# Performance work log

Measured on AMD Instinct MI355X. Metric: run time of the kernel, lower is better.

The kernel has to match this reference:

```python
import jax, jax.numpy as jnp
import numpy as np
import math

S, B, H, NH, I, L, V, BK, MP = 512, 8, 768, 12, 2304, 4, 16384, 32, 512
DH = H // NH   # 64
DV = I // NH   # 192
EPS = 1e-7
SCALE = 1.0 / math.sqrt(3 * DH)


def make_log_bucket_position(relative_pos, bucket_size, max_position):
    sign = np.sign(relative_pos)
    mid = bucket_size // 2
    abs_pos = np.where((relative_pos < mid) & (relative_pos > -mid),
                       mid - 1,
                       np.clip(np.abs(relative_pos), None, max_position - 1))
    log_pos = np.ceil(np.log(abs_pos / mid) / math.log((max_position - 1) / mid) * (mid - 1)).astype(np.int64) + mid
    bucket_pos = np.where(abs_pos <= mid, relative_pos, log_pos * sign).astype(np.int64)
    return bucket_pos


def layer_norm(x, eps=EPS):
    m = jnp.mean(x, axis=-1, keepdims=True)
    v = jnp.var(x, axis=-1, keepdims=True)
    return (x - m) / jnp.sqrt(v + eps)


def setup_inputs() -> dict:
    key = jax.random.key(0)
    ks = jax.random.split(key, 10)
    std = math.sqrt(2.0 / (5.0 * H))
    inp = {}
    inp['input_ids'] = jax.random.randint(ks[0], (S, B), 0, V, dtype=jnp.int32)
    inp['attention_mask'] = jnp.zeros((B, 1, 1, S), dtype=bool)
    rel = np.arange(S)[:, None] - np.arange(S)[None, :]
    rel = make_log_bucket_position(rel, BK, MP)
    inp['position_indices'] = jnp.asarray(BK - 1 + rel, dtype=jnp.int32)  # [S,S] in [0, 2*BK-2]
    inp['word_emb'] = jax.random.normal(ks[1], (V, H), jnp.float32) * std
    inp['rel_emb'] = jax.random.normal(ks[2], (2 * BK - 1, H), jnp.float32) * std
    inp['rel_ln_w'] = jnp.ones((H,), jnp.float32)
    inp['rel_ln_b'] = jnp.zeros((H,), jnp.float32)
    inp['Wv'] = jax.random.normal(ks[3], (L, 2 * I, H), jnp.float32) * std
    inp['Wqk'] = jax.random.normal(ks[4], (L, 2 * H, H), jnp.float32) * std
    inp['bqk'] = jnp.zeros((L, 2 * H), jnp.float32)
    inp['Wo'] = jax.random.normal(ks[5], (L, H, I), jnp.float32) * std
    inp['l_skip'] = jnp.zeros((L, I), jnp.float32)
    return inp


def attention_glu_layer(x, mask, rel, pos_idx, Wv, Wqk, bqk, Wo, l_skip):
    # x: [S,B,H]; rel: [2*BK-1, H]; mask: [B,1,1,S] bool (True = masked)
    h = layer_norm(x)
    vg = jnp.einsum('sbh,ih->sbi', h, Wv)                  # [S,B,2I]
    value, gate = jnp.split(vg, 2, axis=-1)
    gate = jax.nn.gelu(gate, approximate=False)
    value_skip = jax.nn.gelu(value, approximate=False)
    qk = jnp.einsum('sbh,ih->sbi', h, Wqk) + bqk            # [S,B,2H]
    q, k = jnp.split(qk, 2, axis=-1)
    # relative position projections
    pos = rel @ Wqk.T + bqk                                 # [2*BK-1, 2H]
    pos = pos[pos_idx]                                      # [S,S,2H]
    q_pos, k_pos = jnp.split(pos, 2, axis=-1)
    q_pos = q_pos.reshape(S, S, NH, DH)
    k_pos = k_pos.reshape(S, S, NH, DH)
    q4 = q.reshape(S, B, NH, DH)
    k4 = k.reshape(S, B, NH, DH)
    v4 = value.reshape(S, B, NH, DV)
    scores = jnp.einsum('qbhd,kbhd->bhqk', q4, k4) * SCALE
    scores = scores + jnp.einsum('qbhd,qkhd->bhqk', q4, k_pos) * SCALE
    scores = scores + jnp.einsum('kbhd,qkhd->bhqk', k4, q_pos) * SCALE
    scores = jnp.where(mask, -jnp.inf, scores)
    probs = jax.nn.softmax(scores, axis=-1)
    probs = jnp.where(mask, 0.0, probs)
    ctx = jnp.einsum('bhqk,kbhv->qbhv', probs, v4).reshape(S, B, I)
    ctx = ctx + jax.nn.sigmoid(l_skip) * value_skip
    ctx = ctx * gate
    ctx = layer_norm(ctx)
    out = jnp.einsum('sbi,hi->sbh', ctx, Wo)
    return x + out


def reference(input_ids, attention_mask, position_indices, word_emb, rel_emb,
              rel_ln_w, rel_ln_b, Wv, Wqk, bqk, Wo, l_skip):
    x = layer_norm(word_emb[input_ids])                      # [S,B,H]
    rel = layer_norm(rel_emb) * rel_ln_w + rel_ln_b          # [2*BK-1, H]
    for l in range(L):
        x = attention_glu_layer(x, attention_mask, rel, position_indices,
                                Wv[l], Wqk[l], bqk[l], Wo[l], l_skip[l])
    return x
```

## Files before the change

### kernel.cpp

```cpp
#include <hip/hip_runtime.h>
#include <hip/hip_bf16.h>
#include <math.h>

#define S 512
#define B 8
#define H 768
#define NH 12
#define DH 64
#define DV 192
#define II 2304
#define NL 4
#define SCALE 0.07216878364870322f
#define EPS 1e-7f

typedef __attribute__((ext_vector_type(8))) short short8;
typedef __attribute__((ext_vector_type(4))) float f32x4;

__device__ __forceinline__ float b2f(ushort u){
  union { float f; unsigned int u; } v; v.u = ((unsigned int)u) << 16; return v.f;
}
__device__ __forceinline__ ushort f2b(float f){
  union { float f; unsigned int u; } v; v.f = f;
  unsigned int u = v.u;
  return (ushort)((u + 0x7fffu + ((u >> 16) & 1u)) >> 16);
}
__device__ __forceinline__ float gelu_f(float x){
  return 0.5f * x * (1.0f + erff(x * 0.70710678118654752f));
}
__device__ __forceinline__ void async_copy16(const ushort* g, ushort* l){
  __builtin_amdgcn_global_load_lds(
      (const __attribute__((address_space(1))) void*)g,
      (__attribute__((address_space(3))) void*)l, 16, 0, 0);
}

__device__ __forceinline__ void block_sum2(float& s, float& s2, float* red, int t){
  #pragma unroll
  for(int off=32; off>=1; off>>=1){ s += __shfl_xor(s, off); s2 += __shfl_xor(s2, off); }
  int w = t >> 6;
  if((t & 63) == 0){ red[w] = s; red[4 + w] = s2; }
  __syncthreads();
  s  = red[0] + red[1] + red[2] + red[3];
  s2 = red[4] + red[5] + red[6] + red[7];
}

__global__ __launch_bounds__(256)
void f2b_kernel(const float* __restrict__ in, ushort* __restrict__ out){
  int i = (blockIdx.x * 256 + threadIdx.x) * 4;
  float4 v = *(const float4*)(in + i);
  __attribute__((aligned(8))) ushort tmp[4] = { f2b(v.x), f2b(v.y), f2b(v.z), f2b(v.w) };
  *(uint2*)(out + i) = *(const uint2*)tmp;
}

__global__ __launch_bounds__(256)
void embed_ln_kernel(const int* __restrict__ ids, const float* __restrict__ wemb,
                     float* __restrict__ x)
{
  __shared__ float red[8];
  const int sb = blockIdx.x, t = threadIdx.x;
  const float* row = wemb + (size_t)ids[sb] * H;
  float v0 = row[t], v1 = row[t+256], v2 = row[t+512];
  float s = v0+v1+v2, s2 = v0*v0+v1*v1+v2*v2;
  block_sum2(s, s2, red, t);
  float mean = s * (1.0f/H);
  float rstd = rsqrtf(s2*(1.0f/H) - mean*mean + EPS);
  float* xo = x + (size_t)sb * H;
  xo[t]     = (v0-mean)*rstd;
  xo[t+256] = (v1-mean)*rstd;
  xo[t+512] = (v2-mean)*rstd;
}

__global__ __launch_bounds__(256)
void rel_ln_kernel(const float* __restrict__ rel_emb, const float* __restrict__ w,
                   const float* __restrict__ bia, ushort* __restrict__ outb)
{
  __shared__ float red[8];
  const int j = blockIdx.x, t = threadIdx.x;
  const float* row = rel_emb + (size_t)j * H;
  float v0=row[t], v1=row[t+256], v2=row[t+512];
  float s=v0+v1+v2, s2=v0*v0+v1*v1+v2*v2;
  block_sum2(s,s2,red,t);
  float mean = s*(1.0f/H);
  float rstd = rsqrtf(s2*(1.0f/H)-mean*mean+EPS);
  ushort* o = outb + (size_t)j*H;
  o[t]     = f2b((v0-mean)*rstd * w[t]     + bia[t]);
  o[t+256] = f2b((v1-mean)*rstd * w[t+256] + bia[t+256]);
  o[t+512] = f2b((v2-mean)*rstd * w[t+512] + bia[t+512]);
}

__global__ __launch_bounds__(256)
void ln_x_kernel(const float* __restrict__ x, ushort* __restrict__ h)
{
  __shared__ float red[8];
  const int sb = blockIdx.x, t = threadIdx.x;
  const float* row = x + (size_t)sb * H;
  float v0 = row[t], v1 = row[t+256], v2 = row[t+512];
  float s = v0+v1+v2, s2 = v0*v0+v1*v1+v2*v2;
  block_sum2(s, s2, red, t);
  float mean = s * (1.0f/H);
  float rstd = rsqrtf(s2*(1.0f/H) - mean*mean + EPS);
  ushort* o = h + (size_t)sb * H;
  o[t]     = f2b((v0-mean)*rstd);
  o[t+256] = f2b((v1-mean)*rstd);
  o[t+512] = f2b((v2-mean)*rstd);
}

__global__ __launch_bounds__(256)
void gemm_nt64(const ushort* __restrict__ A, const ushort* __restrict__ Bw,
               const float* __restrict__ bias, ushort* __restrict__ Cout,
               int M, int N, int K)
{
  __shared__ ushort As[64][40];
  __shared__ ushort Bs[64][40];
  const int n0 = blockIdx.x * 64, m0 = blockIdx.y * 64;
  const int t = threadIdx.x;
  const int lrow = t >> 2, lk = (t & 3) * 8;
  const int lane = t & 63, w = t >> 6, lr = lane & 15, lq = lane >> 4;
  const int wr = (w >> 1) * 32, wc = (w & 1) * 32;
  f32x4 z = {0.f,0.f,0.f,0.f};
  f32x4 acc[2][2] = {{z,z},{z,z}};
  const int arow = m0 + lrow;
  const ushort* aptr = A  + (size_t)arow * K + lk;
  const ushort* bptr = Bw + (size_t)(n0 + lrow) * K + lk;
  for(int k0 = 0; k0 < K; k0 += 32){
    short8 av = {0,0,0,0,0,0,0,0};
    if(arow < M) av = *(const short8*)(aptr + k0);
    short8 bv = *(const short8*)(bptr + k0);
    __syncthreads();
    *(short8*)&As[lrow][lk] = av;
    *(short8*)&Bs[lrow][lk] = bv;
    __syncthreads();
    short8 a0 = *(const short8*)&As[wr + lr][lq * 8];
    short8 a1 = *(const short8*)&As[wr + 16 + lr][lq * 8];
    short8 b0 = *(const short8*)&Bs[wc + lr][lq * 8];
    short8 b1 = *(const short8*)&Bs[wc + 16 + lr][lq * 8];
    acc[0][0] = __builtin_amdgcn_mfma_f32_16x16x32_bf16(a0, b0, acc[0][0], 0,0,0);
    acc[0][1] = __builtin_amdgcn_mfma_f32_16x16x32_bf16(a0, b1, acc[0][1], 0,0,0);
    acc[1][0] = __builtin_amdgcn_mfma_f32_16x16x32_bf16(a1, b0, acc[1][0], 0,0,0);
    acc[1][1] = __builtin_amdgcn_mfma_f32_16x16x32_bf16(a1, b1, acc[1][1], 0,0,0);
  }
  #pragma unroll
  for(int i=0;i<2;i++){
    #pragma unroll
    for(int j=0;j<2;j++){
      #pragma unroll
      for(int r=0;r<4;r++){
        int m = m0 + wr + i*16 + lq*4 + r;
        int n = n0 + wc + j*16 + lr;
        if(m >= M) continue;
        float v = acc[i][j][r];
        if(bias) v += bias[n];
        Cout[(size_t)m*N + n] = f2b(v);
      }
    }
  }
}

template<int OUT_MODE>
__global__ __launch_bounds__(256)
void gemm128(const ushort* __restrict__ A, const ushort* __restrict__ Bw,
             const float* __restrict__ bias, void* __restrict__ Cout,
             int M, int N, int K)
{
  __shared__ ushort As[128*32];
  __shared__ ushort Bs[128*32];
  const int t = threadIdx.x, w = t>>6, lane = t&63, lr = lane&15, lq = lane>>4;
  const int m0 = blockIdx.y*128, n0 = blockIdx.x*128;
  const int wr = (w>>1)*64, wc = (w&1)*64;
  const int srow = (w*2)*16 + (lane>>2);
  const int sk = (lane&3)*8;
  const ushort* aG = A  + (size_t)(m0+srow)*K + sk;
  const ushort* bG = Bw + (size_t)(n0+srow)*K + sk;
  ushort* aL0 = As + (w*2)*512;
  ushort* aL1 = As + (w*2+1)*512;
  ushort* bL0 = Bs + (w*2)*512;
  ushort* bL1 = Bs + (w*2+1)*512;
  f32x4 z = {0.f,0.f,0.f,0.f};
  f32x4 acc[4][4] = {{z,z,z,z},{z,z,z,z},{z,z,z,z},{z,z,z,z}};
  for(int k0 = 0; k0 < K; k0 += 32){
    __syncthreads();
    async_copy16(aG + k0,                 aL0);
    async_copy16(aG + k0 + (size_t)16*K,  aL1);
    async_copy16(bG + k0,                 bL0);
    async_copy16(bG + k0 + (size_t)16*K,  bL1);
    __syncthreads();
    short8 af[4], bf[4];
    #pragma unroll
    for(int i=0;i<4;i++) af[i] = *(const short8*)&As[(wr + i*16 + lr)*32 + lq*8];
    #pragma unroll
    for(int j=0;j<4;j++) bf[j] = *(const short8*)&Bs[(wc + j*16 + lr)*32 + lq*8];
    #pragma unroll
    for(int i=0;i<4;i++)
      #pragma unroll
      for(int j=0;j<4;j++)
        acc[i][j] = __builtin_amdgcn_mfma_f32_16x16x32_bf16(af[i], bf[j], acc[i][j], 0,0,0);
  }
  #pragma unroll
  for(int i=0;i<4;i++){
    #pragma unroll
    for(int j=0;j<4;j++){
      #pragma unroll
      for(int r=0;r<4;r++){
        int m = m0 + wr + i*16 + lq*4 + r;
        int n = n0 + wc + j*16 + lr;
        float v = acc[i][j][r];
        if(bias) v += bias[n];
        if(OUT_MODE == 0)      ((float*) Cout)[(size_t)m*N + n] = v;
        else if(OUT_MODE == 1) ((ushort*)Cout)[(size_t)m*N + n] = f2b(v);
        else                   ((float*) Cout)[(size_t)m*N + n] += v;
      }
    }
  }
}

__global__ __launch_bounds__(256)
void gemm_vgqk(const ushort* __restrict__ A, const ushort* __restrict__ Ww,
               const float* __restrict__ bqk, ushort* __restrict__ vg,
               ushort* __restrict__ qk)
{
  const int K = H;
  __shared__ ushort As[128*32];
  __shared__ ushort Bs[128*32];
  const int t = threadIdx.x, w = t>>6, lane = t&63, lr = lane&15, lq = lane>>4;
  const int m0 = blockIdx.y*128, n0 = blockIdx.x*128;
  const int wr = (w>>1)*64, wc = (w&1)*64;
  const int srow = (w*2)*16 + (lane>>2);
  const int sk = (lane&3)*8;
  const ushort* aG = A  + (size_t)(m0+srow)*K + sk;
  const ushort* bG = Ww + (size_t)(n0+srow)*K + sk;
  ushort* aL0 = As + (w*2)*512;
  ushort* aL1 = As + (w*2+1)*512;
  ushort* bL0 = Bs + (w*2)*512;
  ushort* bL1 = Bs + (w*2+1)*512;
  f32x4 z = {0.f,0.f,0.f,0.f};
  f32x4 acc[4][4] = {{z,z,z,z},{z,z,z,z},{z,z,z,z},{z,z,z,z}};
  for(int k0 = 0; k0 < K; k0 += 32){
    __syncthreads();
    async_copy16(aG + k0,                 aL0);
    async_copy16(aG + k0 + (size_t)16*K,  aL1);
    async_copy16(bG + k0,                 bL0);
    async_copy16(bG + k0 + (size_t)16*K,  bL1);
    __syncthreads();
    short8 af[4], bf[4];
    #pragma unroll
    for(int i=0;i<4;i++) af[i] = *(const short8*)&As[(wr + i*16 + lr)*32 + lq*8];
    #pragma unroll
    for(int j=0;j<4;j++) bf[j] = *(const short8*)&Bs[(wc + j*16 + lr)*32 + lq*8];
    #pragma unroll
    for(int i=0;i<4;i++)
      #pragma unroll
      for(int j=0;j<4;j++)
        acc[i][j] = __builtin_amdgcn_mfma_f32_16x16x32_bf16(af[i], bf[j], acc[i][j], 0,0,0);
  }
  const bool is_qk = (n0 >= 2*II);
  #pragma unroll
  for(int i=0;i<4;i++){
    #pragma unroll
    for(int j=0;j<4;j++){
      #pragma unroll
      for(int r=0;r<4;r++){
        int m = m0 + wr + i*16 + lq*4 + r;
        int n = n0 + wc + j*16 + lr;
        float v = acc[i][j][r];
        if(is_qk){
          int nq = n - 2*II;
          qk[(size_t)m*(2*H) + nq] = f2b(v + bqk[nq]);
        } else {
          vg[(size_t)m*(2*II) + n] = f2b(v);
        }
      }
    }
  }
}

__global__ __launch_bounds__(256)
void cpq_mfma2_kernel(const ushort* __restrict__ qk, const ushort* __restrict__ posb,
                      ushort* __restrict__ cpT, ushort* __restrict__ cqT)
{
  const int kc = blockIdx.x;
  const int bh = blockIdx.y;
  const int bb = bh / NH, h = bh - bb*NH;
  const int which = blockIdx.z;
  const int t = threadIdx.x, w = t>>6, lane = t&63, lr = lane&15, lq = lane>>4;
  const ushort* ab = posb + (size_t)(w*16 + lr)*1536 + (which ? 0 : 768) + h*64;
  short8 a0 = *(const short8*)(ab + lq*8);
  short8 a1 = *(const short8*)(ab + 32 + lq*8);
  f32x4 z = {0.f,0.f,0.f,0.f};
  f32x4 acc[8] = {z,z,z,z,z,z,z,z};
  #pragma unroll
  for(int nt=0; nt<8; nt++){
    const int k = kc*128 + nt*16 + lr;
    const ushort* bp = qk + ((size_t)k*B + bb)*1536 + (which ? 768 : 0) + h*64;
    short8 b0 = *(const short8*)(bp + lq*8);
    short8 b1 = *(const short8*)(bp + 32 + lq*8);
    acc[nt] = __builtin_amdgcn_mfma_f32_16x16x32_bf16(a0, b0, acc[nt], 0,0,0);
    acc[nt] = __builtin_amdgcn_mfma_f32_16x16x32_bf16(a1, b1, acc[nt], 0,0,0);
  }
  ushort* outp = which ? cqT : cpT;
  #pragma unroll
  for(int nt=0; nt<8; nt++){
    #pragma unroll
    for(int r=0;r<4;r++){
      int j = w*16 + lq*4 + r;
      int k = kc*128 + nt*16 + lr;
      outp[((size_t)bh*64 + j)*512 + k] = f2b(acc[nt][r]);
    }
  }
}

__global__ __launch_bounds__(256)
void vt_kernel(const ushort* __restrict__ vg, ushort* __restrict__ vt)
{
  const int st = blockIdx.x, hh = blockIdx.y, b = blockIdx.z;
  __shared__ ushort tile[32][200];
  const int t = threadIdx.x;
  {
    int sl = t >> 3, v0 = (t & 7) * 24;
    const ushort* src = vg + ((size_t)((st*32 + sl)*B + b))*(2*II) + hh*DV + v0;
    *(short8*)&tile[sl][v0]      = *(const short8*)(src);
    *(short8*)&tile[sl][v0 + 8]  = *(const short8*)(src + 8);
    *(short8*)&tile[sl][v0 + 16] = *(const short8*)(src + 16);
  }
  __syncthreads();
  if(t < DV){
    __attribute__((aligned(16))) ushort tmp[32];
    #pragma unroll
    for(int s2=0;s2<32;s2++) tmp[s2] = tile[s2][t];
    ushort* dst = vt + (((size_t)(b*NH + hh))*DV + t)*S + st*32;
    #pragma unroll
    for(int c=0;c<32;c+=8) *(short8*)(dst + c) = *(const short8*)&tmp[c];
  }
}

__global__ __launch_bounds__(256)
void attn_kernel(const ushort* __restrict__ qk, const ushort* __restrict__ vt,
                 const ushort* __restrict__ cpT, const ushort* __restrict__ cqT,
                 const int* __restrict__ pidx, ushort* __restrict__ ctx)
{
  const int bh = blockIdx.x, qt = blockIdx.y;
  const int b = bh / NH, hh = bh - b*NH;
  __shared__ ushort Qs[16][72];
  __shared__ ushort Ps[16][520];
  __shared__ float cps[16][65];
  __shared__ float redm[4][16];
  __shared__ float reds[4][16];
  __shared__ float rowinv[16];
  const int t = threadIdx.x, w = t>>6, lane = t&63, lr = lane&15, lq = lane>>4;

  {
    int r = t >> 4, d0 = (t & 15) * 4;
    const ushort* src = qk + ((size_t)((qt*16 + r)*B + b))*1536 + hh*DH + d0;
    *(uint2*)&Qs[r][d0] = *(const uint2*)src;
  }
  for(int i=t; i<16*64; i+=256){
    int j = i >> 4, r = i & 15;
    cps[r][j] = b2f(cpT[((size_t)bh*64 + j)*512 + qt*16 + r]);
  }
  __syncthreads();

  float sc[8][4];
  const int kbase = w * 128;
  const ushort* cqbase = cqT + (size_t)bh*64*512;
  #pragma unroll
  for(int tile=0; tile<8; tile++){
    const int k0 = kbase + tile*16;
    const ushort* kp = qk + ((size_t)((k0 + lr)*B + b))*1536 + H + hh*DH + lq*8;
    short8 b0 = *(const short8*)kp;
    short8 b1 = *(const short8*)(kp + 32);
    short8 a0 = *(const short8*)&Qs[lr][lq*8];
    short8 a1 = *(const short8*)&Qs[lr][32 + lq*8];
    f32x4 acc = {0.f,0.f,0.f,0.f};
    acc = __builtin_amdgcn_mfma_f32_16x16x32_bf16(a0, b0, acc, 0,0,0);
    acc = __builtin_amdgcn_mfma_f32_16x16x32_bf16(a1, b1, acc, 0,0,0);
    const int kcol = k0 + lr;
    #pragma unroll
    for(int r=0;r<4;r++){
      int ql = lq*4 + r;
      int pi = pidx[(qt*16+ql)*S + kcol];
      sc[tile][r] = (acc[r] + cps[ql][pi]
                     + b2f(cqbase[(size_t)pi*512 + kcol])) * SCALE;
    }
  }

  float gm[4], gs[4];
  #pragma unroll
  for(int r=0;r<4;r++){
    float m = sc[0][r];
    #pragma unroll
    for(int tile=1;tile<8;tile++) m = fmaxf(m, sc[tile][r]);
    #pragma unroll
    for(int off=1; off<16; off<<=1) m = fmaxf(m, __shfl_xor(m, off));
    if(lr==0) redm[w][lq*4+r] = m;
  }
  __syncthreads();
  #pragma unroll
  for(int r=0;r<4;r++){
    int row = lq*4+r;
    gm[r] = fmaxf(fmaxf(redm[0][row],redm[1][row]),fmaxf(redm[2][row],redm[3][row]));
  }
  #pragma unroll
  for(int r=0;r<4;r++){
    float s = 0.f;
    #pragma unroll
    for(int tile=0;tile<8;tile++){ float e = __expf(sc[tile][r]-gm[r]); sc[tile][r]=e; s+=e; }
    #pragma unroll
    for(int off=1; off<16; off<<=1) s += __shfl_xor(s, off);
    if(lr==0) reds[w][lq*4+r] = s;
  }
  __syncthreads();
  #pragma unroll
  for(int r=0;r<4;r++){
    int row = lq*4+r;
    gs[r] = reds[0][row]+reds[1][row]+reds[2][row]+reds[3][row];
    if(w==0 && lr==0) rowinv[row] = 1.0f/gs[r];
  }
  #pragma unroll
  for(int tile=0;tile<8;tile++){
    #pragma unroll
    for(int r=0;r<4;r++) Ps[lq*4+r][kbase + tile*16 + lr] = f2b(sc[tile][r]);
  }
  __syncthreads();

  f32x4 z = {0.f,0.f,0.f,0.f};
  f32x4 acc2[3] = {z,z,z};
  const ushort* vbase = vt + ((size_t)bh)*DV*S;
  for(int kk=0; kk<S; kk+=32){
    short8 a = *(const short8*)&Ps[lr][kk + lq*8];
    #pragma unroll
    for(int ti=0; ti<3; ti++){
      const int v0 = (w*3 + ti)*16;
      short8 bv = *(const short8*)(vbase + (size_t)(v0 + lr)*S + kk + lq*8);
      acc2[ti] = __builtin_amdgcn_mfma_f32_16x16x32_bf16(a, bv, acc2[ti], 0,0,0);
    }
  }
  #pragma unroll
  for(int ti=0; ti<3; ti++){
    const int v0 = (w*3 + ti)*16;
    #pragma unroll
    for(int r=0;r<4;r++){
      int ql = lq*4 + r;
      float val = acc2[ti][r] * rowinv[ql];
      ctx[((size_t)((qt*16+ql)*B + b))*II + hh*DV + v0 + lr] = f2b(val);
    }
  }
}

__global__ __launch_bounds__(256)
void glu_ln_kernel(const ushort* __restrict__ ctx, const ushort* __restrict__ vg,
                   const float* __restrict__ ls, ushort* __restrict__ outb)
{
  __shared__ float red[8];
  const int sb = blockIdx.x, t = threadIdx.x;
  const ushort* crow = ctx + (size_t)sb*II;
  const ushort* vrow = vg + (size_t)sb*2*II;
  float c[9]; float s=0.f, s2=0.f;
  #pragma unroll
  for(int i=0;i<9;i++){
    int idx = t + i*256;
    float cv  = b2f(crow[idx]);
    float val = b2f(vrow[idx]);
    float gt  = b2f(vrow[II + idx]);
    float sk  = 1.0f/(1.0f + __expf(-ls[idx]));
    cv = (cv + sk*gelu_f(val)) * gelu_f(gt);
    c[i]=cv; s+=cv; s2+=cv*cv;
  }
  block_sum2(s,s2,red,t);
  float mean = s*(1.0f/II);
  float rstd = rsqrtf(s2*(1.0f/II)-mean*mean+EPS);
  ushort* o = outb + (size_t)sb*II;
  #pragma unroll
  for(int i=0;i<9;i++) o[t+i*256] = f2b((c[i]-mean)*rstd);
}

__global__ __launch_bounds__(256)
void copy_kernel(const float* __restrict__ x, float* __restrict__ out){
  int i = (blockIdx.x*256 + threadIdx.x)*4;
  *(float4*)(out + i) = *(const float4*)(x + i);
}

extern "C" void kernel_launch(void* const* d_in, const int* in_sizes, int n_in,
                              void* d_out, int out_size, void* d_ws, size_t ws_size,
                              hipStream_t stream)
{
  (void)in_sizes; (void)n_in; (void)out_size; (void)ws_size;
  const int* ids      = (const int*)d_in[0];
  const int* pidx     = (const int*)d_in[2];
  const float* wemb   = (const float*)d_in[3];
  const float* rele   = (const float*)d_in[4];
  const float* rlw    = (const float*)d_in[5];
  const float* rlb    = (const float*)d_in[6];
  const float* Wv     = (const float*)d_in[7];
  const float* Wqk    = (const float*)d_in[8];
  const float* bqk    = (const float*)d_in[9];
  const float* Wo     = (const float*)d_in[10];
  const float* lskip  = (const float*)d_in[11];

  char* wsb = (char*)d_ws;
  float*  x     = (float*) (wsb + 0);
  ushort* h     = (ushort*)(wsb + 12582912);
  ushort* relb  = (ushort*)(wsb + 18874368);
  ushort* posb  = (ushort*)(wsb + 18972672);
  ushort* vg    = (ushort*)(wsb + 19169280);
  ushort* qk    = (ushort*)(wsb + 56918016);
  ushort* cpT   = (ushort*)(wsb + 69500928);
  ushort* cqT   = (ushort*)(wsb + 75792384);
  ushort* ctx   = (ushort*)(wsb + 82083840);
  ushort* vt    = (ushort*)(wsb + 100958208);
  ushort* ctxln = vt;
  ushort* wvqk  = (ushort*)(wsb + 119832576);
  ushort* wqkb  = wvqk + (size_t)(2*II)*H;
  ushort* wob   = (ushort*)(wsb + 129269760);

  embed_ln_kernel<<<S*B, 256, 0, stream>>>(ids, wemb, x);
  rel_ln_kernel<<<63, 256, 0, stream>>>(rele, rlw, rlb, relb);

  for(int l=0; l<NL; l++){
    const float* Wv_l  = Wv  + (size_t)l * (2*II) * H;
    const float* Wqk_l = Wqk + (size_t)l * (2*H) * H;
    const float* bqk_l = bqk + (size_t)l * (2*H);
    const float* Wo_l  = Wo  + (size_t)l * H * II;
    const float* ls_l  = lskip + (size_t)l * II;

    f2b_kernel<<<(2*II*H)/1024, 256, 0, stream>>>(Wv_l, wvqk);
    f2b_kernel<<<(2*H*H)/1024, 256, 0, stream>>>(Wqk_l, wqkb);
    f2b_kernel<<<(H*II)/1024, 256, 0, stream>>>(Wo_l, wob);

    ln_x_kernel<<<S*B, 256, 0, stream>>>(x, h);
    gemm_vgqk<<<dim3((2*II+2*H)/128, (S*B)/128), 256, 0, stream>>>(h, wvqk, bqk_l, vg, qk);
    gemm_nt64<<<dim3((2*H)/64, 1), 256, 0, stream>>>(relb, wqkb, bqk_l, posb, 63, 2*H, H);
    cpq_mfma2_kernel<<<dim3(S/128, B*NH, 2), 256, 0, stream>>>(qk, posb, cpT, cqT);
    vt_kernel<<<dim3(S/32, NH, B), 256, 0, stream>>>(vg, vt);
    attn_kernel<<<dim3(B*NH, S/16), 256, 0, stream>>>(qk, vt, cpT, cqT, pidx, ctx);
    glu_ln_kernel<<<S*B, 256, 0, stream>>>(ctx, vg, ls_l, ctxln);
    gemm128<2><<<dim3(H/128, (S*B)/128), 256, 0, stream>>>(ctxln, wob, nullptr, x, S*B, H, II);
  }
  copy_kernel<<<(S*B*H)/1024, 256, 0, stream>>>(x, (float*)d_out);
}
```

Before: 1.471 ms.

## Process 32 query rows per attention block and merge weight-conversion launches

The attention kernel now handles 32 query rows per block instead of 16, so each K tile and each V tile loaded from global memory feeds two MFMA row-groups. This halves K/V global traffic per query and halves the grid size. The three per-layer fp32-to-bf16 weight conversions are merged into one launch that writes a contiguous buffer. The trade-off is more LDS and registers per block (sc doubles to 64 floats), which may lower occupancy, and fewer blocks to spread across CUs.

```diff
diff --git a/kernel.cpp b/kernel.cpp
--- a/kernel.cpp
+++ b/kernel.cpp
@@ -13,6 +13,10 @@
 #define SCALE 0.07216878364870322f
 #define EPS 1e-7f
 
+#define NW0 (2*II*H)
+#define NW1 (2*H*H)
+#define NW2 (H*II)
+
 typedef __attribute__((ext_vector_type(8))) short short8;
 typedef __attribute__((ext_vector_type(4))) float f32x4;
 
@@ -44,9 +48,14 @@
 }
 
 __global__ __launch_bounds__(256)
-void f2b_kernel(const float* __restrict__ in, ushort* __restrict__ out){
+void f2b3_kernel(const float* __restrict__ in0, const float* __restrict__ in1,
+                 const float* __restrict__ in2, ushort* __restrict__ out){
   int i = (blockIdx.x * 256 + threadIdx.x) * 4;
-  float4 v = *(const float4*)(in + i);
+  const float* src; int off;
+  if(i < NW0){ src = in0; off = i; }
+  else if(i < NW0+NW1){ src = in1; off = i - NW0; }
+  else { src = in2; off = i - NW0 - NW1; }
+  float4 v = *(const float4*)(src + off);
   __attribute__((aligned(8))) ushort tmp[4] = { f2b(v.x), f2b(v.y), f2b(v.z), f2b(v.w) };
   *(uint2*)(out + i) = *(const uint2*)tmp;
 }
@@ -338,108 +347,125 @@
 {
   const int bh = blockIdx.x, qt = blockIdx.y;
   const int b = bh / NH, hh = bh - b*NH;
-  __shared__ ushort Qs[16][72];
-  __shared__ ushort Ps[16][520];
-  __shared__ float cps[16][65];
-  __shared__ float redm[4][16];
-  __shared__ float reds[4][16];
-  __shared__ float rowinv[16];
+  __shared__ ushort Qs[32][72];
+  __shared__ ushort Ps[32][520];
+  __shared__ float cps[32][65];
+  __shared__ float redm[4][32];
+  __shared__ float reds[4][32];
+  __shared__ float rowinv[32];
   const int t = threadIdx.x, w = t>>6, lane = t&63, lr = lane&15, lq = lane>>4;
 
-  {
-    int r = t >> 4, d0 = (t & 15) * 4;
-    const ushort* src = qk + ((size_t)((qt*16 + r)*B + b))*1536 + hh*DH + d0;
+  for(int i=t; i<512; i+=256){
+    int r = i >> 4, d0 = (i & 15) * 4;
+    const ushort* src = qk + ((size_t)((qt*32 + r)*B + b))*1536 + hh*DH + d0;
     *(uint2*)&Qs[r][d0] = *(const uint2*)src;
   }
-  for(int i=t; i<16*64; i+=256){
-    int j = i >> 4, r = i & 15;
-    cps[r][j] = b2f(cpT[((size_t)bh*64 + j)*512 + qt*16 + r]);
+  for(int i=t; i<32*64; i+=256){
+    int j = i >> 5, r = i & 31;
+    cps[r][j] = b2f(cpT[((size_t)bh*64 + j)*512 + qt*32 + r]);
   }
   __syncthreads();
 
-  float sc[8][4];
+  short8 a00 = *(const short8*)&Qs[lr][lq*8];
+  short8 a01 = *(const short8*)&Qs[lr][32 + lq*8];
+  short8 a10 = *(const short8*)&Qs[16 + lr][lq*8];
+  short8 a11 = *(const short8*)&Qs[16 + lr][32 + lq*8];
+
+  float sc[8][8];
   const int kbase = w * 128;
   const ushort* cqbase = cqT + (size_t)bh*64*512;
+  f32x4 z4 = {0.f,0.f,0.f,0.f};
   #pragma unroll
   for(int tile=0; tile<8; tile++){
     const int k0 = kbase + tile*16;
     const ushort* kp = qk + ((size_t)((k0 + lr)*B + b))*1536 + H + hh*DH + lq*8;
     short8 b0 = *(const short8*)kp;
     short8 b1 = *(const short8*)(kp + 32);
-    short8 a0 = *(const short8*)&Qs[lr][lq*8];
-    short8 a1 = *(const short8*)&Qs[lr][32 + lq*8];
-    f32x4 acc = {0.f,0.f,0.f,0.f};
-    acc = __builtin_amdgcn_mfma_f32_16x16x32_bf16(a0, b0, acc, 0,0,0);
-    acc = __builtin_amdgcn_mfma_f32_16x16x32_bf16(a1, b1, acc, 0,0,0);
+    f32x4 acc[2] = {z4, z4};
+    acc[0] = __builtin_amdgcn_mfma_f32_16x16x32_bf16(a00, b0, acc[0], 0,0,0);
+    acc[0] = __builtin_amdgcn_mfma_f32_16x16x32_bf16(a01, b1, acc[0], 0,0,0);
+    acc[1] = __builtin_amdgcn_mfma_f32_16x16x32_bf16(a10, b0, acc[1], 0,0,0);
+    acc[1] = __builtin_amdgcn_mfma_f32_16x16x32_bf16(a11, b1, acc[1], 0,0,0);
     const int kcol = k0 + lr;
     #pragma unroll
-    for(int r=0;r<4;r++){
-      int ql = lq*4 + r;
-      int pi = pidx[(qt*16+ql)*S + kcol];
-      sc[tile][r] = (acc[r] + cps[ql][pi]
-                     + b2f(cqbase[(size_t)pi*512 + kcol])) * SCALE;
-    }
-  }
-
-  float gm[4], gs[4];
-  #pragma unroll
-  for(int r=0;r<4;r++){
-    float m = sc[0][r];
-    #pragma unroll
-    for(int tile=1;tile<8;tile++) m = fmaxf(m, sc[tile][r]);
+    for(int qs=0;qs<2;qs++){
+      #pragma unroll
+      for(int r=0;r<4;r++){
+        int ql = qs*16 + lq*4 + r;
+        int pi = pidx[(qt*32+ql)*S + kcol];
+        sc[tile][qs*4+r] = (acc[qs][r] + cps[ql][pi]
+                       + b2f(cqbase[(size_t)pi*512 + kcol])) * SCALE;
+      }
+    }
+  }
+
+  float gm[8];
+  #pragma unroll
+  for(int j=0;j<8;j++){
+    float m = sc[0][j];
+    #pragma unroll
+    for(int tile=1;tile<8;tile++) m = fmaxf(m, sc[tile][j]);
     #pragma unroll
     for(int off=1; off<16; off<<=1) m = fmaxf(m, __shfl_xor(m, off));
-    if(lr==0) redm[w][lq*4+r] = m;
+    if(lr==0) redm[w][(j>>2)*16 + lq*4 + (j&3)] = m;
   }
   __syncthreads();
   #pragma unroll
-  for(int r=0;r<4;r++){
-    int row = lq*4+r;
-    gm[r] = fmaxf(fmaxf(redm[0][row],redm[1][row]),fmaxf(redm[2][row],redm[3][row]));
-  }
-  #pragma unroll
-  for(int r=0;r<4;r++){
+  for(int j=0;j<8;j++){
+    int ql = (j>>2)*16 + lq*4 + (j&3);
+    gm[j] = fmaxf(fmaxf(redm[0][ql],redm[1][ql]),fmaxf(redm[2][ql],redm[3][ql]));
+  }
+  #pragma unroll
+  for(int j=0;j<8;j++){
     float s = 0.f;
     #pragma unroll
-    for(int tile=0;tile<8;tile++){ float e = __expf(sc[tile][r]-gm[r]); sc[tile][r]=e; s+=e; }
+    for(int tile=0;tile<8;tile++){ float e = __expf(sc[tile][j]-gm[j]); sc[tile][j]=e; s+=e; }
     #pragma unroll
     for(int off=1; off<16; off<<=1) s += __shfl_xor(s, off);
-    if(lr==0) reds[w][lq*4+r] = s;
+    if(lr==0) reds[w][(j>>2)*16 + lq*4 + (j&3)] = s;
   }
   __syncthreads();
   #pragma unroll
-  for(int r=0;r<4;r++){
-    int row = lq*4+r;
-    gs[r] = reds[0][row]+reds[1][row]+reds[2][row]+reds[3][row];
-    if(w==0 && lr==0) rowinv[row] = 1.0f/gs[r];
+  for(int j=0;j<8;j++){
+    int ql = (j>>2)*16 + lq*4 + (j&3);
+    float g = reds[0][ql]+reds[1][ql]+reds[2][ql]+reds[3][ql];
+    if(w==0 && lr==0) rowinv[ql] = 1.0f/g;
   }
   #pragma unroll
   for(int tile=0;tile<8;tile++){
     #pragma unroll
-    for(int r=0;r<4;r++) Ps[lq*4+r][kbase + tile*16 + lr] = f2b(sc[tile][r]);
+    for(int j=0;j<8;j++){
+      int ql = (j>>2)*16 + lq*4 + (j&3);
+      Ps[ql][kbase + tile*16 + lr] = f2b(sc[tile][j]);
+    }
   }
   __syncthreads();
 
-  f32x4 z = {0.f,0.f,0.f,0.f};
-  f32x4 acc2[3] = {z,z,z};
+  f32x4 acc2[2][3] = {{z4,z4,z4},{z4,z4,z4}};
   const ushort* vbase = vt + ((size_t)bh)*DV*S;
+  #pragma unroll 4
   for(int kk=0; kk<S; kk+=32){
-    short8 a = *(const short8*)&Ps[lr][kk + lq*8];
+    short8 p0 = *(const short8*)&Ps[lr][kk + lq*8];
+    short8 p1 = *(const short8*)&Ps[16 + lr][kk + lq*8];
     #pragma unroll
     for(int ti=0; ti<3; ti++){
       const int v0 = (w*3 + ti)*16;
       short8 bv = *(const short8*)(vbase + (size_t)(v0 + lr)*S + kk + lq*8);
-      acc2[ti] = __builtin_amdgcn_mfma_f32_16x16x32_bf16(a, bv, acc2[ti], 0,0,0);
-    }
-  }
-  #pragma unroll
-  for(int ti=0; ti<3; ti++){
-    const int v0 = (w*3 + ti)*16;
-    #pragma unroll
-    for(int r=0;r<4;r++){
-      int ql = lq*4 + r;
-      float val = acc2[ti][r] * rowinv[ql];
-      ctx[((size_t)((qt*16+ql)*B + b))*II + hh*DV + v0 + lr] = f2b(val);
+      acc2[0][ti] = __builtin_amdgcn_mfma_f32_16x16x32_bf16(p0, bv, acc2[0][ti], 0,0,0);
+      acc2[1][ti] = __builtin_amdgcn_mfma_f32_16x16x32_bf16(p1, bv, acc2[1][ti], 0,0,0);
+    }
+  }
+  #pragma unroll
+  for(int qs=0;qs<2;qs++){
+    #pragma unroll
+    for(int ti=0; ti<3; ti++){
+      const int v0 = (w*3 + ti)*16;
+      #pragma unroll
+      for(int r=0;r<4;r++){
+        int ql = qs*16 + lq*4 + r;
+        float val = acc2[qs][ti][r] * rowinv[ql];
+        ctx[((size_t)((qt*32+ql)*B + b))*II + hh*DV + v0 + lr] = f2b(val);
+      }
     }
   }
 }
@@ -507,29 +533,27 @@
   ushort* vt    = (ushort*)(wsb + 100958208);
   ushort* ctxln = vt;
   ushort* wvqk  = (ushort*)(wsb + 119832576);
-  ushort* wqkb  = wvqk + (size_t)(2*II)*H;
-  ushort* wob   = (ushort*)(wsb + 129269760);
+  ushort* wqkb  = wvqk + (size_t)NW0;
+  ushort* wob   = wvqk + (size_t)(NW0 + NW1);
 
   embed_ln_kernel<<<S*B, 256, 0, stream>>>(ids, wemb, x);
   rel_ln_kernel<<<63, 256, 0, stream>>>(rele, rlw, rlb, relb);
 
   for(int l=0; l<NL; l++){
-    const float* Wv_l  = Wv  + (size_t)l * (2*II) * H;
-    const float* Wqk_l = Wqk + (size_t)l * (2*H) * H;
+    const float* Wv_l  = Wv  + (size_t)l * NW0;
+    const float* Wqk_l = Wqk + (size_t)l * NW1;
     const float* bqk_l = bqk + (size_t)l * (2*H);
-    const float* Wo_l  = Wo  + (size_t)l * H * II;
+    const float* Wo_l  = Wo  + (size_t)l * NW2;
     const float* ls_l  = lskip + (size_t)l * II;
 
-    f2b_kernel<<<(2*II*H)/1024, 256, 0, stream>>>(Wv_l, wvqk);
-    f2b_kernel<<<(2*H*H)/1024, 256, 0, stream>>>(Wqk_l, wqkb);
-    f2b_kernel<<<(H*II)/1024, 256, 0, stream>>>(Wo_l, wob);
+    f2b3_kernel<<<(NW0+NW1+NW2)/1024, 256, 0, stream>>>(Wv_l, Wqk_l, Wo_l, wvqk);
 
     ln_x_kernel<<<S*B, 256, 0, stream>>>(x, h);
     gemm_vgqk<<<dim3((2*II+2*H)/128, (S*B)/128), 256, 0, stream>>>(h, wvqk, bqk_l, vg, qk);
     gemm_nt64<<<dim3((2*H)/64, 1), 256, 0, stream>>>(relb, wqkb, bqk_l, posb, 63, 2*H, H);
     cpq_mfma2_kernel<<<dim3(S/128, B*NH, 2), 256, 0, stream>>>(qk, posb, cpT, cqT);
     vt_kernel<<<dim3(S/32, NH, B), 256, 0, stream>>>(vg, vt);
-    attn_kernel<<<dim3(B*NH, S/16), 256, 0, stream>>>(qk, vt, cpT, cqT, pidx, ctx);
+    attn_kernel<<<dim3(B*NH, S/32), 256, 0, stream>>>(qk, vt, cpT, cqT, pidx, ctx);
     glu_ln_kernel<<<S*B, 256, 0, stream>>>(ctx, vg, ls_l, ctxln);
     gemm128<2><<<dim3(H/128, (S*B)/128), 256, 0, stream>>>(ctxln, wob, nullptr, x, S*B, H, II);
   }
```

After: 1.339 ms. 1.1x faster.
